# Optimization experiments

Hardware: AMD Instinct MI355X
Metric: run time of the kernel (lower is better)

## Reference

```python
import jax, jax.numpy as jnp
import numpy as np

KH, KW, PAD, DIL, STRIDE = 3, 3, 1, 1, 1


def _conv2d(x, w):
    # plain dense conv, NCHW / OIHW, stride 1, pad 1
    return jax.lax.conv_general_dilated(
        x, w, window_strides=(STRIDE, STRIDE),
        padding=[(PAD, PAD), (PAD, PAD)],
        rhs_dilation=(DIL, DIL),
        dimension_numbers=('NCHW', 'OIHW', 'NCHW'))


def _deform_patches(x, offset):
    """Bilinear-sample deformable patches.
    x: [B,C,H,W], offset: [B,2K,Ho,Wo] with per-tap (dy,dx).
    Returns [B,C,K,Ho,Wo]."""
    B, C, H, W = x.shape
    Ho, Wo = offset.shape[2], offset.shape[3]
    K = KH * KW
    off = offset.reshape(B, K, 2, Ho, Wo)

    ky = jnp.repeat(jnp.arange(KH), KW)            # [K]
    kx = jnp.tile(jnp.arange(KW), KH)              # [K]
    base_y = (jnp.arange(Ho) * STRIDE - PAD)[None, :, None] + (DIL * ky)[:, None, None]  # [K,Ho,1]
    base_x = (jnp.arange(Wo) * STRIDE - PAD)[None, None, :] + (DIL * kx)[:, None, None]  # [K,1,Wo]

    sy = base_y[None].astype(x.dtype) + off[:, :, 0]   # [B,K,Ho,Wo]
    sx = base_x[None].astype(x.dtype) + off[:, :, 1]

    y0 = jnp.floor(sy); x0 = jnp.floor(sx)
    ly = sy - y0;       lx = sx - x0
    y0i = y0.astype(jnp.int32); x0i = x0.astype(jnp.int32)

    x_flat = x.reshape(B, C, H * W)

    def corner(yi, xi, wgt):
        valid = (yi >= 0) & (yi < H) & (xi >= 0) & (xi < W)   # zero padding outside
        idx = (jnp.clip(yi, 0, H - 1) * W + jnp.clip(xi, 0, W - 1))  # [B,K,Ho,Wo]
        gath = jax.vmap(lambda img, i: img[:, i.reshape(-1)])(x_flat, idx)  # [B,C,K*Ho*Wo]
        gath = gath.reshape(B, C, K, Ho, Wo)
        return gath * (wgt * valid.astype(x.dtype))[:, None]

    p = corner(y0i,     x0i,     (1 - ly) * (1 - lx))
    p = p + corner(y0i,     x0i + 1, (1 - ly) * lx)
    p = p + corner(y0i + 1, x0i,     ly * (1 - lx))
    p = p + corner(y0i + 1, x0i + 1, ly * lx)
    return p  # [B,C,K,Ho,Wo]


def setup_inputs() -> dict:
    key = jax.random.key(0)
    k1, k2, k3 = jax.random.split(key, 3)
    B, C, H, W = 8, 256, 64, 64
    Cout = 256
    x = jax.random.normal(k1, (B, C, H, W), dtype=jnp.float32)
    offset_w = jax.random.normal(k2, (2 * KH * KW, C, KH, KW), dtype=jnp.float32) * 0.02
    deform_w = jax.random.normal(k3, (Cout, C, KH, KW), dtype=jnp.float32) * 0.02
    return {"x": x, "offset_w": offset_w, "deform_w": deform_w}


def reference(x, offset_w, deform_w):
    # 1) offset-predicting conv
    offset = _conv2d(x, offset_w)                    # [B,2K,H,W]
    # 2) deformable conv = bilinear gather + contraction over (Cin, K)
    patches = _deform_patches(x, offset)             # [B,C,K,H,W]
    Cout = deform_w.shape[0]
    wk = deform_w.reshape(Cout, deform_w.shape[1], KH * KW)
    y = jnp.einsum('bckhw,ock->bohw', patches, wk)   # [B,Cout,H,W]
    # 3) avg + std channel attention (torch.std default: unbiased, ddof=1)
    avg = jnp.mean(y, axis=(2, 3), keepdims=True)
    std = jnp.std(y, axis=(2, 3), keepdims=True, ddof=1)
    attn = jax.nn.sigmoid(avg + std)
    return y * attn
```

## Files before the change

kernel.cpp:

```cpp
#include <hip/hip_runtime.h>
#include <hip/hip_bf16.h>
#include <math.h>

#define C_IN 256
#define H_   64
#define W_   64
#define B_   8
#define COUT 256
#define HW   (H_*W_)

typedef float f32x4 __attribute__((ext_vector_type(4)));
typedef short short8 __attribute__((ext_vector_type(8)));

static __device__ __forceinline__ int pack_bf16x2(float a, float b) {
    __hip_bfloat162 h = __float22bfloat162_rn(make_float2(a, b));
    union { __hip_bfloat162 h; int i; } u; u.h = h;
    return u.i;
}

static __device__ __forceinline__ void unpk(int v, float& lo, float& hi) {
    union { int i; float f; } a, b;
    a.i = v << 16;
    b.i = v & 0xffff0000;
    lo = a.f; hi = b.f;
}

__global__ __launch_bounds__(256) void prep_weights_kernel(
    const float* __restrict__ ow, const float* __restrict__ dw,
    short* __restrict__ wR, short* __restrict__ wO)
{
    int blk = blockIdx.x;
    int k   = blk / 288;
    int row = blk % 288;
    int c   = threadIdx.x;
    union { float f; unsigned u; } a;
    if (row < 256) {
        a.f = dw[(size_t)row * 2304 + c * 9 + k];
        unsigned r = (a.u + 0x7fffu + ((a.u >> 16) & 1u)) >> 16;
        wR[(size_t)k * 65536 + row * 256 + c] = (short)r;
    } else {
        int o = row - 256;
        a.f = (o < 18) ? ow[(size_t)o * 2304 + c * 9 + k] : 0.f;
        unsigned r = (a.u + 0x7fffu + ((a.u >> 16) & 1u)) >> 16;
        wO[(size_t)k * 8192 + o * 256 + c] = (short)r;
    }
}

__global__ __launch_bounds__(256) void transpose_x_kernel(
    const float* __restrict__ x, unsigned short* __restrict__ xT)
{
    __shared__ float tile[64][257];
    const int tid = threadIdx.x;
    const int b = blockIdx.x >> 6, h = blockIdx.x & 63;
    const float* xb = x + ((size_t)b << 20) + h * 64;

#pragma unroll
    for (int pass = 0; pass < 16; ++pass) {
        int c  = pass * 16 + (tid >> 4);
        int w0 = (tid & 15) * 4;
        float4 v = *(const float4*)(xb + (size_t)c * 4096 + w0);
        tile[w0][c] = v.x; tile[w0 + 1][c] = v.y;
        tile[w0 + 2][c] = v.z; tile[w0 + 3][c] = v.w;
    }
    __syncthreads();

    int4* ob = (int4*)(xT + ((size_t)blockIdx.x << 14));
#pragma unroll
    for (int pass = 0; pass < 8; ++pass) {
        int idx = pass * 256 + tid;
        int w = idx >> 5, ch8 = idx & 31;
        const float* tr = &tile[w][ch8 * 8];
        int4 pk;
        pk.x = pack_bf16x2(tr[0], tr[1]);
        pk.y = pack_bf16x2(tr[2], tr[3]);
        pk.z = pack_bf16x2(tr[4], tr[5]);
        pk.w = pack_bf16x2(tr[6], tr[7]);
        ob[idx] = pk;
    }
}

__global__ __launch_bounds__(256, 2) void offset_mfma_kernel(
    const unsigned short* __restrict__ xT, const short* __restrict__ wO,
    float* __restrict__ offs)
{
    __shared__ int4 aT[32 * 8];
    __shared__ int4 bT[64 * 8];

    const int tid = threadIdx.x;
    const int b   = blockIdx.x & 7;
    const int ho  = blockIdx.x >> 3;

    const int px = tid >> 2;
    const int cg = tid & 3;
    const int wv = tid >> 6;
    const int ln = tid & 63;
    const int lo = ln & 15;
    const int quad = ln >> 4;

    f32x4 acc[2];
    acc[0] = (f32x4){0.f, 0.f, 0.f, 0.f};
    acc[1] = (f32x4){0.f, 0.f, 0.f, 0.f};

    const unsigned short* xbb = xT + ((size_t)b << 20);
    const int oA = tid >> 3, octA = tid & 7;
    const int4 zero4 = {0, 0, 0, 0};

    for (int s = 0; s < 36; ++s) {
        int k  = s >> 2;
        int c0 = (s & 3) << 6;
        int yy = ho + k / 3 - 1;
        int xx = px + k % 3 - 1;
        bool valid = (yy >= 0) & (yy < 64) & (xx >= 0) & (xx < 64);
        int yc = min(max(yy, 0), 63), xc = min(max(xx, 0), 63);

        const int4* src = (const int4*)(xbb + (((size_t)yc * 64 + xc) << 8) + c0 + cg * 16);
        int4 p0 = valid ? src[0] : zero4;
        int4 p1 = valid ? src[1] : zero4;
        bT[px * 8 + ((2 * cg)     ^ (px & 7))] = p0;
        bT[px * 8 + ((2 * cg + 1) ^ (px & 7))] = p1;

        aT[oA * 8 + (octA ^ (oA & 7))] =
            *(const int4*)(wO + (size_t)k * 8192 + oA * 256 + c0 + octA * 8);
        __syncthreads();

        int pxl = wv * 16 + lo;
#pragma unroll
        for (int ks = 0; ks < 2; ++ks) {
            int ch = ks * 4 + quad;
            short8 bfr = *(const short8*)&bT[pxl * 8 + (ch ^ (pxl & 7))];
#pragma unroll
            for (int t = 0; t < 2; ++t) {
                int o = t * 16 + lo;
                short8 afr = *(const short8*)&aT[o * 8 + (ch ^ (o & 7))];
                acc[t] = __builtin_amdgcn_mfma_f32_16x16x32_bf16(afr, bfr, acc[t], 0, 0, 0);
            }
        }
        __syncthreads();
    }

#pragma unroll
    for (int t = 0; t < 2; ++t) {
#pragma unroll
        for (int r = 0; r < 4; ++r) {
            int o = t * 16 + quad * 4 + r;
            if (o < 18)
                offs[((size_t)b * 18 + o) * HW + ho * 64 + wv * 16 + lo] = acc[t][r];
        }
    }
}

__global__ __launch_bounds__(256, 2) void deform_mfma_kernel(
    const unsigned short* __restrict__ xT, const float* __restrict__ offs,
    const short* __restrict__ wR, float* __restrict__ y,
    float* __restrict__ sum_, float* __restrict__ sumsq_)
{
    __shared__ int4   meta_i[576];
    __shared__ float4 meta_w[576];
    __shared__ int4   aT[256 * 8];
    __shared__ int4   bT[64 * 8];

    const int tid = threadIdx.x;
    const int b   = blockIdx.x & 7;
    const int ho  = blockIdx.x >> 3;

    for (int e = tid; e < 576; e += 256) {
        int kk = e >> 6;
        int pxe = e & 63;
        float dy = offs[((size_t)b * 18 + 2 * kk)     * HW + ho * W_ + pxe];
        float dx = offs[((size_t)b * 18 + 2 * kk + 1) * HW + ho * W_ + pxe];
        float sy = (float)(ho - 1 + kk / 3) + dy;
        float sx = (float)(pxe - 1 + kk % 3) + dx;
        float y0f = floorf(sy), x0f = floorf(sx);
        float ly = sy - y0f, lx = sx - x0f;
        int y0 = (int)y0f, x0 = (int)x0f;
        int y1 = y0 + 1, x1 = x0 + 1;
        float wy0 = 1.f - ly, wy1 = ly, wx0 = 1.f - lx, wx1 = lx;
        bool vy0 = (y0 >= 0) & (y0 < H_), vy1 = (y1 >= 0) & (y1 < H_);
        bool vx0 = (x0 >= 0) & (x0 < W_), vx1 = (x1 >= 0) & (x1 < W_);
        int cy0 = min(max(y0, 0), H_ - 1), cy1 = min(max(y1, 0), H_ - 1);
        int cx0 = min(max(x0, 0), W_ - 1), cx1 = min(max(x1, 0), W_ - 1);
        int4 ii; float4 ww;
        ii.x = cy0 * W_ + cx0;  ww.x = wy0 * wx0 * ((vy0 & vx0) ? 1.f : 0.f);
        ii.y = cy0 * W_ + cx1;  ww.y = wy0 * wx1 * ((vy0 & vx1) ? 1.f : 0.f);
        ii.z = cy1 * W_ + cx0;  ww.z = wy1 * wx0 * ((vy1 & vx0) ? 1.f : 0.f);
        ii.w = cy1 * W_ + cx1;  ww.w = wy1 * wx1 * ((vy1 & vx1) ? 1.f : 0.f);
        meta_i[e] = ii;
        meta_w[e] = ww;
    }

    const int px = tid >> 2;
    const int cg = tid & 3;
    const int wv = tid >> 6;
    const int ln = tid & 63;
    const int lo = ln & 15;
    const int quad = ln >> 4;

    f32x4 acc[4][4];
#pragma unroll
    for (int t = 0; t < 4; ++t)
#pragma unroll
        for (int p = 0; p < 4; ++p)
            acc[t][p] = (f32x4){0.f, 0.f, 0.f, 0.f};

    const unsigned short* xbb = xT + ((size_t)b << 20) + cg * 16;
    const int oA = tid >> 3, octA = tid & 7;

    __syncthreads();

    for (int s = 0; s < 36; ++s) {
        int k  = s >> 2;
        int c0 = (s & 3) << 6;

        int4   ii = meta_i[k * 64 + px];
        float4 ww = meta_w[k * 64 + px];

        const unsigned short* xc0 = xbb + c0;
        const int4* pA = (const int4*)(xc0 + ((size_t)ii.x << 8));
        const int4* pB = (const int4*)(xc0 + ((size_t)ii.y << 8));
        const int4* pC = (const int4*)(xc0 + ((size_t)ii.z << 8));
        const int4* pD = (const int4*)(xc0 + ((size_t)ii.w << 8));
        int4 a0 = pA[0], a1 = pA[1];
        int4 b0 = pB[0], b1 = pB[1];
        int4 cc0 = pC[0], cc1 = pC[1];
        int4 d0 = pD[0], d1 = pD[1];

        auto blend = [&](int av, int bv, int cv, int dv) -> int {
            float alo, ahi, blo, bhi, clo, chi, dlo, dhi;
            unpk(av, alo, ahi); unpk(bv, blo, bhi);
            unpk(cv, clo, chi); unpk(dv, dlo, dhi);
            float vlo = ww.x * alo + ww.y * blo + ww.z * clo + ww.w * dlo;
            float vhi = ww.x * ahi + ww.y * bhi + ww.z * chi + ww.w * dhi;
            return pack_bf16x2(vlo, vhi);
        };
        int4 o0, o1;
        o0.x = blend(a0.x, b0.x, cc0.x, d0.x);
        o0.y = blend(a0.y, b0.y, cc0.y, d0.y);
        o0.z = blend(a0.z, b0.z, cc0.z, d0.z);
        o0.w = blend(a0.w, b0.w, cc0.w, d0.w);
        o1.x = blend(a1.x, b1.x, cc1.x, d1.x);
        o1.y = blend(a1.y, b1.y, cc1.y, d1.y);
        o1.z = blend(a1.z, b1.z, cc1.z, d1.z);
        o1.w = blend(a1.w, b1.w, cc1.w, d1.w);
        bT[px * 8 + ((2 * cg)     ^ (px & 7))] = o0;
        bT[px * 8 + ((2 * cg + 1) ^ (px & 7))] = o1;

        const short* wk = wR + (size_t)k * 65536 + c0;
#pragma unroll
        for (int it = 0; it < 8; ++it) {
            int o = oA + it * 32;
            aT[o * 8 + (octA ^ (o & 7))] = *(const int4*)(wk + o * 256 + octA * 8);
        }
        __syncthreads();

#pragma unroll
        for (int ks = 0; ks < 2; ++ks) {
            int ch = ks * 4 + quad;
            short8 afr[4], bfr[4];
#pragma unroll
            for (int t = 0; t < 4; ++t) {
                int o = wv * 64 + t * 16 + lo;
                afr[t] = *(const short8*)&aT[o * 8 + (ch ^ (o & 7))];
                int p = t * 16 + lo;
                bfr[t] = *(const short8*)&bT[p * 8 + (ch ^ (p & 7))];
            }
#pragma unroll
            for (int t = 0; t < 4; ++t)
#pragma unroll
                for (int p = 0; p < 4; ++p)
                    acc[t][p] = __builtin_amdgcn_mfma_f32_16x16x32_bf16(
                        afr[t], bfr[p], acc[t][p], 0, 0, 0);
        }
        __syncthreads();
    }

    float* yb = y + ((size_t)b << 20) + ho * 64;
#pragma unroll
    for (int t = 0; t < 4; ++t) {
#pragma unroll
        for (int r = 0; r < 4; ++r) {
            int o = wv * 64 + t * 16 + quad * 4 + r;
            float sv = 0.f, qv = 0.f;
#pragma unroll
            for (int p = 0; p < 4; ++p) {
                float val = acc[t][p][r];
                yb[(size_t)o * HW + p * 16 + lo] = val;
                sv += val;
                qv += val * val;
            }
#pragma unroll
            for (int m = 1; m <= 8; m <<= 1) {
                sv += __shfl_xor(sv, m, 16);
                qv += __shfl_xor(qv, m, 16);
            }
            if (lo == 0) {
                atomicAdd(&sum_[b * COUT + o], sv);
                atomicAdd(&sumsq_[b * COUT + o], qv);
            }
        }
    }
}

__global__ __launch_bounds__(256) void attn_scale_kernel(
    const float* __restrict__ sum_, const float* __restrict__ sumsq_,
    float* __restrict__ y)
{
    int bo = blockIdx.x;
    float s = sum_[bo], q = sumsq_[bo];
    float mean = s * (1.f / 4096.f);
    float var  = (q - s * s * (1.f / 4096.f)) * (1.f / 4095.f);
    float sd   = sqrtf(fmaxf(var, 0.f));
    float attn = 1.f / (1.f + expf(-(mean + sd)));
    float4* yp = (float4*)(y + (size_t)bo * HW);
#pragma unroll
    for (int i = 0; i < 4; ++i) {
        float4 v = yp[threadIdx.x + i * 256];
        v.x *= attn; v.y *= attn; v.z *= attn; v.w *= attn;
        yp[threadIdx.x + i * 256] = v;
    }
}

extern "C" void kernel_launch(void* const* d_in, const int* in_sizes, int n_in,
                              void* d_out, int out_size, void* d_ws, size_t ws_size,
                              hipStream_t stream)
{
    const float* x  = (const float*)d_in[0];
    const float* ow = (const float*)d_in[1];
    const float* dw = (const float*)d_in[2];
    float* out = (float*)d_out;
    float* ws  = (float*)d_ws;

    float*          offs = ws;
    unsigned short* xT   = (unsigned short*)(ws + 589824);
    short*          wR   = (short*)(xT + 8388608);
    short*          wO   = wR + 589824;
    float*          sum_ = (float*)(wO + 73728);
    float*          sumsq_ = sum_ + 2048;

    hipMemsetAsync(sum_, 0, 2 * 2048 * sizeof(float), stream);

    prep_weights_kernel<<<9 * 288, 256, 0, stream>>>(ow, dw, wR, wO);
    transpose_x_kernel<<<512, 256, 0, stream>>>(x, xT);
    offset_mfma_kernel<<<512, 256, 0, stream>>>(xT, wO, offs);
    deform_mfma_kernel<<<512, 256, 0, stream>>>(xT, offs, wR, out, sum_, sumsq_);
    attn_scale_kernel<<<2048, 256, 0, stream>>>(sum_, sumsq_, out);
}
```

Before: 198.2 us.

## Load MFMA weight fragments directly from global and double-buffer deform gather

The deform kernel no longer stages weights through shared memory. Each wave loads its A fragments straight from global with nontemporal loads. The bilinear-gathered B tile is double-buffered in LDS, so the gather and blend for the next step overlap the MFMAs of the current one, and only one barrier per step remains. The offset kernel likewise drops LDS staging and loads fragments directly, with higher occupancy bounds. The step order is changed to channel-major, and bf16 packing now uses a manual rounding routine. The risks are higher register pressure from prefetch registers and redundant global weight reads across waves.

```diff
diff --git a/kernel.cpp b/kernel.cpp
--- a/kernel.cpp
+++ b/kernel.cpp
@@ -10,19 +10,28 @@
 #define HW   (H_*W_)
 
 typedef float f32x4 __attribute__((ext_vector_type(4)));
+typedef float f32x2 __attribute__((ext_vector_type(2)));
 typedef short short8 __attribute__((ext_vector_type(8)));
+typedef int   i32x4 __attribute__((ext_vector_type(4)));
+
+union cvt8 { i32x4 v; short8 s; };
 
 static __device__ __forceinline__ int pack_bf16x2(float a, float b) {
-    __hip_bfloat162 h = __float22bfloat162_rn(make_float2(a, b));
-    union { __hip_bfloat162 h; int i; } u; u.h = h;
-    return u.i;
-}
-
-static __device__ __forceinline__ void unpk(int v, float& lo, float& hi) {
+    union { float f; unsigned u; } x, y;
+    x.f = a; y.f = b;
+    unsigned lo = (x.u + 0x7fffu + ((x.u >> 16) & 1u)) >> 16;
+    unsigned hi = (y.u + 0x7fffu + ((y.u >> 16) & 1u)) & 0xffff0000u;
+    return (int)(lo | hi);
+}
+
+static __device__ __forceinline__ f32x2 up2(int v) {
     union { int i; float f; } a, b;
-    a.i = v << 16;
-    b.i = v & 0xffff0000;
-    lo = a.f; hi = b.f;
+    a.i = v << 16; b.i = v & 0xffff0000;
+    return (f32x2){a.f, b.f};
+}
+
+static __device__ __forceinline__ int pk2(f32x2 r) {
+    return pack_bf16x2(r[0], r[1]);
 }
 
 __global__ __launch_bounds__(256) void prep_weights_kernel(
@@ -51,8 +60,7 @@
 {
     __shared__ float tile[64][257];
     const int tid = threadIdx.x;
-    const int b = blockIdx.x >> 6, h = blockIdx.x & 63;
-    const float* xb = x + ((size_t)b << 20) + h * 64;
+    const float* xb = x + ((size_t)(blockIdx.x >> 6) << 20) + (blockIdx.x & 63) * 64;
 
 #pragma unroll
     for (int pass = 0; pass < 16; ++pass) {
@@ -79,63 +87,58 @@
     }
 }
 
-__global__ __launch_bounds__(256, 2) void offset_mfma_kernel(
+__global__ __launch_bounds__(256, 4) void offset_mfma_kernel(
     const unsigned short* __restrict__ xT, const short* __restrict__ wO,
     float* __restrict__ offs)
 {
-    __shared__ int4 aT[32 * 8];
-    __shared__ int4 bT[64 * 8];
-
     const int tid = threadIdx.x;
     const int b   = blockIdx.x & 7;
     const int ho  = blockIdx.x >> 3;
 
-    const int px = tid >> 2;
-    const int cg = tid & 3;
     const int wv = tid >> 6;
     const int ln = tid & 63;
     const int lo = ln & 15;
     const int quad = ln >> 4;
+    const int pxl = wv * 16 + lo;
 
     f32x4 acc[2];
     acc[0] = (f32x4){0.f, 0.f, 0.f, 0.f};
     acc[1] = (f32x4){0.f, 0.f, 0.f, 0.f};
 
     const unsigned short* xbb = xT + ((size_t)b << 20);
-    const int oA = tid >> 3, octA = tid & 7;
-    const int4 zero4 = {0, 0, 0, 0};
+    const i32x4 z4 = {0, 0, 0, 0};
 
     for (int s = 0; s < 36; ++s) {
-        int k  = s >> 2;
-        int c0 = (s & 3) << 6;
+        int c4 = s / 9, k = s - c4 * 9, c0 = c4 << 6;
         int yy = ho + k / 3 - 1;
-        int xx = px + k % 3 - 1;
+        int xx = pxl + k % 3 - 1;
         bool valid = (yy >= 0) & (yy < 64) & (xx >= 0) & (xx < 64);
         int yc = min(max(yy, 0), 63), xc = min(max(xx, 0), 63);
-
-        const int4* src = (const int4*)(xbb + (((size_t)yc * 64 + xc) << 8) + c0 + cg * 16);
-        int4 p0 = valid ? src[0] : zero4;
-        int4 p1 = valid ? src[1] : zero4;
-        bT[px * 8 + ((2 * cg)     ^ (px & 7))] = p0;
-        bT[px * 8 + ((2 * cg + 1) ^ (px & 7))] = p1;
-
-        aT[oA * 8 + (octA ^ (oA & 7))] =
-            *(const int4*)(wO + (size_t)k * 8192 + oA * 256 + c0 + octA * 8);
-        __syncthreads();
-
-        int pxl = wv * 16 + lo;
+        const unsigned short* src = xbb + (((size_t)yc * 64 + xc) << 8) + c0 + quad * 8;
+
+        i32x4 bf[2];
+#pragma unroll
+        for (int ks = 0; ks < 2; ++ks)
+            bf[ks] = valid ? *(const i32x4*)(src + ks * 32) : z4;
+
+        const short* wb = wO + k * 8192 + lo * 256 + c0 + quad * 8;
+        i32x4 af[2][2];
+#pragma unroll
+        for (int t = 0; t < 2; ++t)
+#pragma unroll
+            for (int ks = 0; ks < 2; ++ks)
+                af[t][ks] = __builtin_nontemporal_load(
+                    (const i32x4*)(wb + t * 4096 + ks * 32));
+
 #pragma unroll
         for (int ks = 0; ks < 2; ++ks) {
-            int ch = ks * 4 + quad;
-            short8 bfr = *(const short8*)&bT[pxl * 8 + (ch ^ (pxl & 7))];
+            cvt8 bb; bb.v = bf[ks];
 #pragma unroll
             for (int t = 0; t < 2; ++t) {
-                int o = t * 16 + lo;
-                short8 afr = *(const short8*)&aT[o * 8 + (ch ^ (o & 7))];
-                acc[t] = __builtin_amdgcn_mfma_f32_16x16x32_bf16(afr, bfr, acc[t], 0, 0, 0);
-            }
-        }
-        __syncthreads();
+                cvt8 aa; aa.v = af[t][ks];
+                acc[t] = __builtin_amdgcn_mfma_f32_16x16x32_bf16(aa.s, bb.s, acc[t], 0, 0, 0);
+            }
+        }
     }
 
 #pragma unroll
@@ -144,20 +147,19 @@
         for (int r = 0; r < 4; ++r) {
             int o = t * 16 + quad * 4 + r;
             if (o < 18)
-                offs[((size_t)b * 18 + o) * HW + ho * 64 + wv * 16 + lo] = acc[t][r];
-        }
-    }
-}
-
-__global__ __launch_bounds__(256, 2) void deform_mfma_kernel(
+                offs[((size_t)b * 18 + o) * HW + ho * 64 + pxl] = acc[t][r];
+        }
+    }
+}
+
+__global__ __launch_bounds__(256, 3) void deform_mfma_kernel(
     const unsigned short* __restrict__ xT, const float* __restrict__ offs,
     const short* __restrict__ wR, float* __restrict__ y,
     float* __restrict__ sum_, float* __restrict__ sumsq_)
 {
     __shared__ int4   meta_i[576];
     __shared__ float4 meta_w[576];
-    __shared__ int4   aT[256 * 8];
-    __shared__ int4   bT[64 * 8];
+    __shared__ int4   bT[2][64 * 8];
 
     const int tid = threadIdx.x;
     const int b   = blockIdx.x & 7;
@@ -203,74 +205,99 @@
             acc[t][p] = (f32x4){0.f, 0.f, 0.f, 0.f};
 
     const unsigned short* xbb = xT + ((size_t)b << 20) + cg * 16;
-    const int oA = tid >> 3, octA = tid & 7;
+    const int bwr = px * 8;
+    const int sw0 = (2 * cg)     ^ (px & 7);
+    const int sw1 = (2 * cg + 1) ^ (px & 7);
 
     __syncthreads();
 
+    int4   cr[8];
+    float4 wwp;
+    {
+        int4 ii = meta_i[px];
+        wwp = meta_w[px];
+        const int4* pA = (const int4*)(xbb + ((size_t)ii.x << 8));
+        const int4* pB = (const int4*)(xbb + ((size_t)ii.y << 8));
+        const int4* pC = (const int4*)(xbb + ((size_t)ii.z << 8));
+        const int4* pD = (const int4*)(xbb + ((size_t)ii.w << 8));
+        cr[0] = pA[0]; cr[1] = pA[1];
+        cr[2] = pB[0]; cr[3] = pB[1];
+        cr[4] = pC[0]; cr[5] = pC[1];
+        cr[6] = pD[0]; cr[7] = pD[1];
+        int4 o0, o1;
+        o0.x = pk2(wwp.x * up2(cr[0].x) + wwp.y * up2(cr[2].x) + wwp.z * up2(cr[4].x) + wwp.w * up2(cr[6].x));
+        o0.y = pk2(wwp.x * up2(cr[0].y) + wwp.y * up2(cr[2].y) + wwp.z * up2(cr[4].y) + wwp.w * up2(cr[6].y));
+        o0.z = pk2(wwp.x * up2(cr[0].z) + wwp.y * up2(cr[2].z) + wwp.z * up2(cr[4].z) + wwp.w * up2(cr[6].z));
+        o0.w = pk2(wwp.x * up2(cr[0].w) + wwp.y * up2(cr[2].w) + wwp.z * up2(cr[4].w) + wwp.w * up2(cr[6].w));
+        o1.x = pk2(wwp.x * up2(cr[1].x) + wwp.y * up2(cr[3].x) + wwp.z * up2(cr[5].x) + wwp.w * up2(cr[7].x));
+        o1.y = pk2(wwp.x * up2(cr[1].y) + wwp.y * up2(cr[3].y) + wwp.z * up2(cr[5].y) + wwp.w * up2(cr[7].y));
+        o1.z = pk2(wwp.x * up2(cr[1].z) + wwp.y * up2(cr[3].z) + wwp.z * up2(cr[5].z) + wwp.w * up2(cr[7].z));
+        o1.w = pk2(wwp.x * up2(cr[1].w) + wwp.y * up2(cr[3].w) + wwp.z * up2(cr[5].w) + wwp.w * up2(cr[7].w));
+        bT[0][bwr + sw0] = o0;
+        bT[0][bwr + sw1] = o1;
+    }
+
+#pragma unroll 2
     for (int s = 0; s < 36; ++s) {
-        int k  = s >> 2;
-        int c0 = (s & 3) << 6;
-
-        int4   ii = meta_i[k * 64 + px];
-        float4 ww = meta_w[k * 64 + px];
-
-        const unsigned short* xc0 = xbb + c0;
-        const int4* pA = (const int4*)(xc0 + ((size_t)ii.x << 8));
-        const int4* pB = (const int4*)(xc0 + ((size_t)ii.y << 8));
-        const int4* pC = (const int4*)(xc0 + ((size_t)ii.z << 8));
-        const int4* pD = (const int4*)(xc0 + ((size_t)ii.w << 8));
-        int4 a0 = pA[0], a1 = pA[1];
-        int4 b0 = pB[0], b1 = pB[1];
-        int4 cc0 = pC[0], cc1 = pC[1];
-        int4 d0 = pD[0], d1 = pD[1];
-
-        auto blend = [&](int av, int bv, int cv, int dv) -> int {
-            float alo, ahi, blo, bhi, clo, chi, dlo, dhi;
-            unpk(av, alo, ahi); unpk(bv, blo, bhi);
-            unpk(cv, clo, chi); unpk(dv, dlo, dhi);
-            float vlo = ww.x * alo + ww.y * blo + ww.z * clo + ww.w * dlo;
-            float vhi = ww.x * ahi + ww.y * bhi + ww.z * chi + ww.w * dhi;
-            return pack_bf16x2(vlo, vhi);
-        };
-        int4 o0, o1;
-        o0.x = blend(a0.x, b0.x, cc0.x, d0.x);
-        o0.y = blend(a0.y, b0.y, cc0.y, d0.y);
-        o0.z = blend(a0.z, b0.z, cc0.z, d0.z);
-        o0.w = blend(a0.w, b0.w, cc0.w, d0.w);
-        o1.x = blend(a1.x, b1.x, cc1.x, d1.x);
-        o1.y = blend(a1.y, b1.y, cc1.y, d1.y);
-        o1.z = blend(a1.z, b1.z, cc1.z, d1.z);
-        o1.w = blend(a1.w, b1.w, cc1.w, d1.w);
-        bT[px * 8 + ((2 * cg)     ^ (px & 7))] = o0;
-        bT[px * 8 + ((2 * cg + 1) ^ (px & 7))] = o1;
-
-        const short* wk = wR + (size_t)k * 65536 + c0;
-#pragma unroll
-        for (int it = 0; it < 8; ++it) {
-            int o = oA + it * 32;
-            aT[o * 8 + (octA ^ (o & 7))] = *(const int4*)(wk + o * 256 + octA * 8);
-        }
         __syncthreads();
+        int c4 = s / 9, k = s - c4 * 9, c0 = c4 << 6;
+
+        const short* wb = wR + k * 65536 + (wv * 64 + lo) * 256 + c0 + quad * 8;
+        i32x4 aL[4][2];
+#pragma unroll
+        for (int t = 0; t < 4; ++t)
+#pragma unroll
+            for (int ks = 0; ks < 2; ++ks)
+                aL[t][ks] = __builtin_nontemporal_load(
+                    (const i32x4*)(wb + t * 4096 + ks * 32));
+
+        if (s < 35) {
+            int s1 = s + 1;
+            int c41 = s1 / 9, k1 = s1 - c41 * 9, c01 = c41 << 6;
+            int4 ii = meta_i[k1 * 64 + px];
+            wwp = meta_w[k1 * 64 + px];
+            const unsigned short* xc = xbb + c01;
+            const int4* pA = (const int4*)(xc + ((size_t)ii.x << 8));
+            const int4* pB = (const int4*)(xc + ((size_t)ii.y << 8));
+            const int4* pC = (const int4*)(xc + ((size_t)ii.z << 8));
+            const int4* pD = (const int4*)(xc + ((size_t)ii.w << 8));
+            cr[0] = pA[0]; cr[1] = pA[1];
+            cr[2] = pB[0]; cr[3] = pB[1];
+            cr[4] = pC[0]; cr[5] = pC[1];
+            cr[6] = pD[0]; cr[7] = pD[1];
+        }
 
 #pragma unroll
         for (int ks = 0; ks < 2; ++ks) {
-            int ch = ks * 4 + quad;
-            short8 afr[4], bfr[4];
+            short8 bfr[4];
+#pragma unroll
+            for (int p = 0; p < 4; ++p) {
+                int pr = p * 16 + lo;
+                bfr[p] = *(const short8*)&bT[s & 1][pr * 8 + ((ks * 4 + quad) ^ (pr & 7))];
+            }
 #pragma unroll
             for (int t = 0; t < 4; ++t) {
-                int o = wv * 64 + t * 16 + lo;
-                afr[t] = *(const short8*)&aT[o * 8 + (ch ^ (o & 7))];
-                int p = t * 16 + lo;
-                bfr[t] = *(const short8*)&bT[p * 8 + (ch ^ (p & 7))];
-            }
-#pragma unroll
-            for (int t = 0; t < 4; ++t)
+                cvt8 aa; aa.v = aL[t][ks];
 #pragma unroll
                 for (int p = 0; p < 4; ++p)
                     acc[t][p] = __builtin_amdgcn_mfma_f32_16x16x32_bf16(
-                        afr[t], bfr[p], acc[t][p], 0, 0, 0);
-        }
-        __syncthreads();
+                        aa.s, bfr[p], acc[t][p], 0, 0, 0);
+            }
+        }
+
+        if (s < 35) {
+            int4 o0, o1;
+            o0.x = pk2(wwp.x * up2(cr[0].x) + wwp.y * up2(cr[2].x) + wwp.z * up2(cr[4].x) + wwp.w * up2(cr[6].x));
+            o0.y = pk2(wwp.x * up2(cr[0].y) + wwp.y * up2(cr[2].y) + wwp.z * up2(cr[4].y) + wwp.w * up2(cr[6].y));
+            o0.z = pk2(wwp.x * up2(cr[0].z) + wwp.y * up2(cr[2].z) + wwp.z * up2(cr[4].z) + wwp.w * up2(cr[6].z));
+            o0.w = pk2(wwp.x * up2(cr[0].w) + wwp.y * up2(cr[2].w) + wwp.z * up2(cr[4].w) + wwp.w * up2(cr[6].w));
+            o1.x = pk2(wwp.x * up2(cr[1].x) + wwp.y * up2(cr[3].x) + wwp.z * up2(cr[5].x) + wwp.w * up2(cr[7].x));
+            o1.y = pk2(wwp.x * up2(cr[1].y) + wwp.y * up2(cr[3].y) + wwp.z * up2(cr[5].y) + wwp.w * up2(cr[7].y));
+            o1.z = pk2(wwp.x * up2(cr[1].z) + wwp.y * up2(cr[3].z) + wwp.z * up2(cr[5].z) + wwp.w * up2(cr[7].z));
+            o1.w = pk2(wwp.x * up2(cr[1].w) + wwp.y * up2(cr[3].w) + wwp.z * up2(cr[5].w) + wwp.w * up2(cr[7].w));
+            bT[(s + 1) & 1][bwr + sw0] = o0;
+            bT[(s + 1) & 1][bwr + sw1] = o1;
+        }
     }
 
     float* yb = y + ((size_t)b << 20) + ho * 64;
```

New measurement: 277.2 us. 39.9% more time.
